# Kernel tuning notes

Measured on AMD Instinct MI355X. Metric: run time of the kernel, lower is better.

The kernel has to match this reference:

```python
import jax, jax.numpy as jnp
import numpy as np

INPUT_SIZE = 4096
OUTPUT_SIZE = 4096
N = 6  # LUT fan-in -> 2^N = 64 entries per LUT
BATCH = 2048


def setup_inputs() -> dict:
    key = jax.random.key(0)
    kx, km, kl = jax.random.split(key, 3)
    # binary input bits stored as float32 {0,1}
    x = jax.random.randint(kx, (BATCH, INPUT_SIZE), 0, 2).astype(jnp.float32)
    # 'random' layer mapping: each of the OUTPUT_SIZE LUTs reads N input bit positions
    mapping = jax.random.randint(km, (OUTPUT_SIZE, N), 0, INPUT_SIZE).astype(jnp.int32)
    # LUT weights, uniform in [-1, 1] as in torch init (clamped to [-1,1] anyway)
    luts = jax.random.uniform(kl, (OUTPUT_SIZE, 2 ** N), dtype=jnp.float32) * 2.0 - 1.0
    return {"x": x, "mapping": mapping, "luts": luts}


def _lut_forward(x, mapping, luts):
    # clamp_luts (training-time clamp, applied in-place in torch forward)
    luts = jnp.clip(luts, -1.0, 1.0)
    n = mapping.shape[1]
    # gather the selected input bits: (B, O, n)
    selected = x[:, mapping]
    # pack bits into a LUT address: (B, O)
    powers = (2 ** jnp.arange(n, dtype=jnp.int32)).astype(x.dtype)
    addresses = (selected * powers).sum(axis=-1).astype(jnp.int32)
    # second gather: per-output LUT lookup -> (B, O)
    out = luts[jnp.arange(luts.shape[0], dtype=jnp.int32)[None, :], addresses]
    # STE binarization (forward: hard threshold > 0)
    binary = (out > 0).astype(out.dtype)
    return out + jax.lax.stop_gradient(binary - out) if False else binary  # fwd-only: hard output


def reference(x, mapping, luts):
    return _lut_forward(x, mapping, luts)
```

## Files before the change

### kernel.cpp

```cpp
#include <hip/hip_runtime.h>
#include <stdint.h>


static constexpr int IN    = 4096;
static constexpr int OUTW  = 4096;
static constexpr int BATCH = 2048;

__global__ __launch_bounds__(256) void prep_kernel(const float* __restrict__ x,
                                                   const float* __restrict__ luts,
                                                   uint32_t* __restrict__ xbits,
                                                   unsigned long long* __restrict__ lut_pos) {
    if (blockIdx.x < 256) {
        const int g = blockIdx.x >> 2;
        const int chunk = blockIdx.x & 3;
        const int m = chunk * 1024 + threadIdx.x * 4;
        const float* xb = x + ((size_t)g * 32) * IN + m;
        uint32_t v0 = 0, v1 = 0, v2 = 0, v3 = 0;
#pragma unroll
        for (int r = 0; r < 32; ++r) {
            const float4 f = *(const float4*)(xb + (size_t)r * IN);
            v0 |= ((uint32_t)(f.x != 0.0f)) << r;
            v1 |= ((uint32_t)(f.y != 0.0f)) << r;
            v2 |= ((uint32_t)(f.z != 0.0f)) << r;
            v3 |= ((uint32_t)(f.w != 0.0f)) << r;
        }
        *(uint4*)(xbits + (size_t)g * IN + m) = make_uint4(v0, v1, v2, v3);
    } else {
        const int wave = threadIdx.x >> 6;
        const int lane = threadIdx.x & 63;
        const int base = (blockIdx.x - 256) * 128 + wave * 32;
#pragma unroll
        for (int i = 0; i < 32; i += 4) {
            const float v0 = luts[(size_t)(base + i + 0) * 64 + lane];
            const float v1 = luts[(size_t)(base + i + 1) * 64 + lane];
            const float v2 = luts[(size_t)(base + i + 2) * 64 + lane];
            const float v3 = luts[(size_t)(base + i + 3) * 64 + lane];
            const unsigned long long m0 = __ballot(v0 > 0.0f);
            const unsigned long long m1 = __ballot(v1 > 0.0f);
            const unsigned long long m2 = __ballot(v2 > 0.0f);
            const unsigned long long m3 = __ballot(v3 > 0.0f);
            if (lane == 0) {
                lut_pos[base + i + 0] = m0;
                lut_pos[base + i + 1] = m1;
                lut_pos[base + i + 2] = m2;
                lut_pos[base + i + 3] = m3;
            }
        }
    }
}

__global__ __launch_bounds__(256) void lut_fwd_kernel(const int* __restrict__ mapping,
                                                      const uint32_t* __restrict__ xbits,
                                                      const unsigned long long* __restrict__ lut_pos,
                                                      float* __restrict__ out) {
    __shared__ uint32_t sbits[IN];
    const int g  = blockIdx.x & 63;
    const int cb = blockIdx.x >> 6;
    {
        const uint4* src = (const uint4*)(xbits + (size_t)g * IN);
        uint4* dst = (uint4*)sbits;
#pragma unroll
        for (int i = 0; i < 4; ++i) dst[threadIdx.x + i * 256] = src[threadIdx.x + i * 256];
    }
    __syncthreads();

    const int j = cb * 512 + threadIdx.x * 2;
    const int4* mrow = (const int4*)(mapping + (size_t)j * 6);
    const int4 q0 = mrow[0];
    const int4 q1 = mrow[1];
    const int4 q2 = mrow[2];

    const uint32_t w00 = sbits[q0.x], w01 = sbits[q0.y], w02 = sbits[q0.z],
                   w03 = sbits[q0.w], w04 = sbits[q1.x], w05 = sbits[q1.y];
    const uint32_t w10 = sbits[q1.z], w11 = sbits[q1.w], w12 = sbits[q2.x],
                   w13 = sbits[q2.y], w14 = sbits[q2.z], w15 = sbits[q2.w];
    const ulonglong2 masks = *(const ulonglong2*)(lut_pos + j);

    float* outp = out + ((size_t)g * 32) * OUTW + j;
#pragma unroll
    for (int r = 0; r < 32; ++r) {
        const uint32_t a0 = ((w00 >> r) & 1u)        | (((w01 >> r) & 1u) << 1)
                          | (((w02 >> r) & 1u) << 2) | (((w03 >> r) & 1u) << 3)
                          | (((w04 >> r) & 1u) << 4) | (((w05 >> r) & 1u) << 5);
        const uint32_t a1 = ((w10 >> r) & 1u)        | (((w11 >> r) & 1u) << 1)
                          | (((w12 >> r) & 1u) << 2) | (((w13 >> r) & 1u) << 3)
                          | (((w14 >> r) & 1u) << 4) | (((w15 >> r) & 1u) << 5);
        float2 res;
        res.x = (float)((uint32_t)(masks.x >> a0) & 1u);
        res.y = (float)((uint32_t)(masks.y >> a1) & 1u);
        *(float2*)(outp + (size_t)r * OUTW) = res;
    }
}

__global__ __launch_bounds__(256) void naive_kernel(const float* __restrict__ x,
                                                    const int* __restrict__ mapping,
                                                    const float* __restrict__ luts,
                                                    float* __restrict__ out) {
    const int idx = blockIdx.x * 256 + threadIdx.x;
    const int b = idx >> 12;
    const int j = idx & (OUTW - 1);
    const float* xr = x + (size_t)b * IN;
    int addr = 0;
#pragma unroll
    for (int k = 0; k < 6; ++k) {
        addr |= ((int)(xr[mapping[j * 6 + k]] != 0.0f)) << k;
    }
    out[idx] = (luts[j * 64 + addr] > 0.0f) ? 1.0f : 0.0f;
}

extern "C" void kernel_launch(void* const* d_in, const int* in_sizes, int n_in,
                              void* d_out, int out_size, void* d_ws, size_t ws_size,
                              hipStream_t stream) {
    const float* x       = (const float*)d_in[0];
    const int*   mapping = (const int*)d_in[1];
    const float* luts    = (const float*)d_in[2];
    float* out = (float*)d_out;

    const size_t lut_pos_bytes = (size_t)OUTW * 8;
    const size_t xbits_bytes   = (size_t)64 * IN * 4;
    if (ws_size >= lut_pos_bytes + xbits_bytes) {
        unsigned long long* lut_pos = (unsigned long long*)d_ws;
        uint32_t* xbits = (uint32_t*)((char*)d_ws + lut_pos_bytes);
        hipLaunchKernelGGL(prep_kernel, dim3(288), dim3(256), 0, stream,
                           x, luts, xbits, lut_pos);
        hipLaunchKernelGGL(lut_fwd_kernel, dim3(512), dim3(256), 0, stream,
                           mapping, xbits, lut_pos, out);
    } else {
        hipLaunchKernelGGL(naive_kernel, dim3((BATCH * OUTW) / 256), dim3(256), 0, stream,
                           x, mapping, luts, out);
    }
}
```

Measured before the change: 91.48 us.

## Fuse bit-packing, LUT mask prep and lookup into a single kernel

Replaces the prep kernel plus lookup kernel with one kernel. Each block packs its batch group's input bits and computes the LUT sign masks for its output chunk directly into shared memory, then produces its outputs with nontemporal stores. This removes the second launch and the workspace round-trip. In exchange, each batch group's x slice is re-read by four blocks, LUT data is recomputed per block, and the grid is small (256 blocks of 512 threads).

```diff
diff --git a/kernel.cpp b/kernel.cpp
--- a/kernel.cpp
+++ b/kernel.cpp
@@ -6,14 +6,23 @@
 static constexpr int OUTW  = 4096;
 static constexpr int BATCH = 2048;
 
-__global__ __launch_bounds__(256) void prep_kernel(const float* __restrict__ x,
-                                                   const float* __restrict__ luts,
-                                                   uint32_t* __restrict__ xbits,
-                                                   unsigned long long* __restrict__ lut_pos) {
-    if (blockIdx.x < 256) {
-        const int g = blockIdx.x >> 2;
-        const int chunk = blockIdx.x & 3;
-        const int m = chunk * 1024 + threadIdx.x * 4;
+typedef float vfloat2 __attribute__((ext_vector_type(2)));
+
+__global__ __launch_bounds__(512) void fused_kernel(const float* __restrict__ x,
+                                                    const int* __restrict__ mapping,
+                                                    const float* __restrict__ luts,
+                                                    float* __restrict__ out) {
+    __shared__ uint32_t sbits[IN];
+    __shared__ unsigned long long smask[1024];
+
+    const int bid  = blockIdx.x;
+    const int slot = bid >> 3;
+    const int g    = (bid & 7) * 8 + (slot >> 2);
+    const int cb   = slot & 3;
+
+#pragma unroll
+    for (int c = 0; c < 2; ++c) {
+        const int m = c * 2048 + threadIdx.x * 4;
         const float* xb = x + ((size_t)g * 32) * IN + m;
         uint32_t v0 = 0, v1 = 0, v2 = 0, v3 = 0;
 #pragma unroll
@@ -24,47 +33,36 @@
             v2 |= ((uint32_t)(f.z != 0.0f)) << r;
             v3 |= ((uint32_t)(f.w != 0.0f)) << r;
         }
-        *(uint4*)(xbits + (size_t)g * IN + m) = make_uint4(v0, v1, v2, v3);
-    } else {
-        const int wave = threadIdx.x >> 6;
-        const int lane = threadIdx.x & 63;
-        const int base = (blockIdx.x - 256) * 128 + wave * 32;
+        *(uint4*)(sbits + m) = make_uint4(v0, v1, v2, v3);
+    }
+
+    {
+        const int wave  = threadIdx.x >> 6;
+        const int lane  = threadIdx.x & 63;
+        const int cbase = wave * 128;
+        const float* lp = luts + ((size_t)(cb * 1024 + cbase)) * 64 + lane;
 #pragma unroll
-        for (int i = 0; i < 32; i += 4) {
-            const float v0 = luts[(size_t)(base + i + 0) * 64 + lane];
-            const float v1 = luts[(size_t)(base + i + 1) * 64 + lane];
-            const float v2 = luts[(size_t)(base + i + 2) * 64 + lane];
-            const float v3 = luts[(size_t)(base + i + 3) * 64 + lane];
+        for (int i = 0; i < 128; i += 4) {
+            const float v0 = lp[(size_t)(i + 0) * 64];
+            const float v1 = lp[(size_t)(i + 1) * 64];
+            const float v2 = lp[(size_t)(i + 2) * 64];
+            const float v3 = lp[(size_t)(i + 3) * 64];
             const unsigned long long m0 = __ballot(v0 > 0.0f);
             const unsigned long long m1 = __ballot(v1 > 0.0f);
             const unsigned long long m2 = __ballot(v2 > 0.0f);
             const unsigned long long m3 = __ballot(v3 > 0.0f);
             if (lane == 0) {
-                lut_pos[base + i + 0] = m0;
-                lut_pos[base + i + 1] = m1;
-                lut_pos[base + i + 2] = m2;
-                lut_pos[base + i + 3] = m3;
+                smask[cbase + i + 0] = m0;
+                smask[cbase + i + 1] = m1;
+                smask[cbase + i + 2] = m2;
+                smask[cbase + i + 3] = m3;
             }
         }
     }
-}
-
-__global__ __launch_bounds__(256) void lut_fwd_kernel(const int* __restrict__ mapping,
-                                                      const uint32_t* __restrict__ xbits,
-                                                      const unsigned long long* __restrict__ lut_pos,
-                                                      float* __restrict__ out) {
-    __shared__ uint32_t sbits[IN];
-    const int g  = blockIdx.x & 63;
-    const int cb = blockIdx.x >> 6;
-    {
-        const uint4* src = (const uint4*)(xbits + (size_t)g * IN);
-        uint4* dst = (uint4*)sbits;
-#pragma unroll
-        for (int i = 0; i < 4; ++i) dst[threadIdx.x + i * 256] = src[threadIdx.x + i * 256];
-    }
     __syncthreads();
 
-    const int j = cb * 512 + threadIdx.x * 2;
+    const int jl = threadIdx.x * 2;
+    const int j  = cb * 1024 + jl;
     const int4* mrow = (const int4*)(mapping + (size_t)j * 6);
     const int4 q0 = mrow[0];
     const int4 q1 = mrow[1];
@@ -74,7 +72,8 @@
                    w03 = sbits[q0.w], w04 = sbits[q1.x], w05 = sbits[q1.y];
     const uint32_t w10 = sbits[q1.z], w11 = sbits[q1.w], w12 = sbits[q2.x],
                    w13 = sbits[q2.y], w14 = sbits[q2.z], w15 = sbits[q2.w];
-    const ulonglong2 masks = *(const ulonglong2*)(lut_pos + j);
+    const unsigned long long mk0 = smask[jl];
+    const unsigned long long mk1 = smask[jl + 1];
 
     float* outp = out + ((size_t)g * 32) * OUTW + j;
 #pragma unroll
@@ -85,27 +84,11 @@
         const uint32_t a1 = ((w10 >> r) & 1u)        | (((w11 >> r) & 1u) << 1)
                           | (((w12 >> r) & 1u) << 2) | (((w13 >> r) & 1u) << 3)
                           | (((w14 >> r) & 1u) << 4) | (((w15 >> r) & 1u) << 5);
-        float2 res;
-        res.x = (float)((uint32_t)(masks.x >> a0) & 1u);
-        res.y = (float)((uint32_t)(masks.y >> a1) & 1u);
-        *(float2*)(outp + (size_t)r * OUTW) = res;
+        vfloat2 res;
+        res.x = (float)((uint32_t)(mk0 >> a0) & 1u);
+        res.y = (float)((uint32_t)(mk1 >> a1) & 1u);
+        __builtin_nontemporal_store(res, (vfloat2*)(outp + (size_t)r * OUTW));
     }
-}
-
-__global__ __launch_bounds__(256) void naive_kernel(const float* __restrict__ x,
-                                                    const int* __restrict__ mapping,
-                                                    const float* __restrict__ luts,
-                                                    float* __restrict__ out) {
-    const int idx = blockIdx.x * 256 + threadIdx.x;
-    const int b = idx >> 12;
-    const int j = idx & (OUTW - 1);
-    const float* xr = x + (size_t)b * IN;
-    int addr = 0;
-#pragma unroll
-    for (int k = 0; k < 6; ++k) {
-        addr |= ((int)(xr[mapping[j * 6 + k]] != 0.0f)) << k;
-    }
-    out[idx] = (luts[j * 64 + addr] > 0.0f) ? 1.0f : 0.0f;
 }
 
 extern "C" void kernel_launch(void* const* d_in, const int* in_sizes, int n_in,
@@ -115,18 +98,8 @@
     const int*   mapping = (const int*)d_in[1];
     const float* luts    = (const float*)d_in[2];
     float* out = (float*)d_out;
+    (void)d_ws; (void)ws_size;
 
-    const size_t lut_pos_bytes = (size_t)OUTW * 8;
-    const size_t xbits_bytes   = (size_t)64 * IN * 4;
-    if (ws_size >= lut_pos_bytes + xbits_bytes) {
-        unsigned long long* lut_pos = (unsigned long long*)d_ws;
-        uint32_t* xbits = (uint32_t*)((char*)d_ws + lut_pos_bytes);
-        hipLaunchKernelGGL(prep_kernel, dim3(288), dim3(256), 0, stream,
-                           x, luts, xbits, lut_pos);
-        hipLaunchKernelGGL(lut_fwd_kernel, dim3(512), dim3(256), 0, stream,
-                           mapping, xbits, lut_pos, out);
-    } else {
-        hipLaunchKernelGGL(naive_kernel, dim3((BATCH * OUTW) / 256), dim3(256), 0, stream,
-                           x, mapping, luts, out);
-    }
+    hipLaunchKernelGGL(fused_kernel, dim3(256), dim3(512), 0, stream,
+                       x, mapping, luts, out);
 }
```

After: 99.43 us. 1.09x slower.

## Fuse x bit-packing into main kernel, 4 rows per block, nontemporal IO

Applied to the files above, without the earlier changes.

Moves the packing of input bits into the main kernel. Each block now packs 4 batch rows straight into shared memory, which removes the xbits workspace round trip and its separate launch. The LUT sign-mask prep becomes its own small kernel. Each thread now handles 4 outputs per row with float4 nontemporal stores and nontemporal loads of x. The trade-off is that every block now reloads all 4096 mapping entries and lut masks for only 4 rows, where before it reused them across 32 rows, so mapping and mask traffic per output rises.

```diff
diff --git a/kernel.cpp b/kernel.cpp
--- a/kernel.cpp
+++ b/kernel.cpp
@@ -6,89 +6,102 @@
 static constexpr int OUTW  = 4096;
 static constexpr int BATCH = 2048;
 
-__global__ __launch_bounds__(256) void prep_kernel(const float* __restrict__ x,
-                                                   const float* __restrict__ luts,
-                                                   uint32_t* __restrict__ xbits,
-                                                   unsigned long long* __restrict__ lut_pos) {
-    if (blockIdx.x < 256) {
-        const int g = blockIdx.x >> 2;
-        const int chunk = blockIdx.x & 3;
-        const int m = chunk * 1024 + threadIdx.x * 4;
-        const float* xb = x + ((size_t)g * 32) * IN + m;
+typedef float vfloat4 __attribute__((ext_vector_type(4)));
+
+__global__ __launch_bounds__(256) void lutprep_kernel(const float* __restrict__ luts,
+                                                      unsigned long long* __restrict__ lut_pos) {
+    const int wave = threadIdx.x >> 6;
+    const int lane = threadIdx.x & 63;
+    const int base = blockIdx.x * 256 + wave * 64;
+#pragma unroll
+    for (int i = 0; i < 64; i += 4) {
+        const float v0 = luts[(size_t)(base + i + 0) * 64 + lane];
+        const float v1 = luts[(size_t)(base + i + 1) * 64 + lane];
+        const float v2 = luts[(size_t)(base + i + 2) * 64 + lane];
+        const float v3 = luts[(size_t)(base + i + 3) * 64 + lane];
+        const unsigned long long m0 = __ballot(v0 > 0.0f);
+        const unsigned long long m1 = __ballot(v1 > 0.0f);
+        const unsigned long long m2 = __ballot(v2 > 0.0f);
+        const unsigned long long m3 = __ballot(v3 > 0.0f);
+        if (lane == 0) {
+            lut_pos[base + i + 0] = m0;
+            lut_pos[base + i + 1] = m1;
+            lut_pos[base + i + 2] = m2;
+            lut_pos[base + i + 3] = m3;
+        }
+    }
+}
+
+__global__ __launch_bounds__(256) void lut_main_kernel(const float* __restrict__ x,
+                                                       const int* __restrict__ mapping,
+                                                       const unsigned long long* __restrict__ lut_pos,
+                                                       float* __restrict__ out) {
+    __shared__ uint32_t sbits[IN];
+    const int g = blockIdx.x;
+    const int t = threadIdx.x;
+
+#pragma unroll
+    for (int c = 0; c < 4; ++c) {
+        const int m = c * 1024 + t * 4;
+        const float* xb = x + ((size_t)g * 4) * IN + m;
         uint32_t v0 = 0, v1 = 0, v2 = 0, v3 = 0;
 #pragma unroll
-        for (int r = 0; r < 32; ++r) {
-            const float4 f = *(const float4*)(xb + (size_t)r * IN);
+        for (int r = 0; r < 4; ++r) {
+            const vfloat4 f = __builtin_nontemporal_load((const vfloat4*)(xb + (size_t)r * IN));
             v0 |= ((uint32_t)(f.x != 0.0f)) << r;
             v1 |= ((uint32_t)(f.y != 0.0f)) << r;
             v2 |= ((uint32_t)(f.z != 0.0f)) << r;
             v3 |= ((uint32_t)(f.w != 0.0f)) << r;
         }
-        *(uint4*)(xbits + (size_t)g * IN + m) = make_uint4(v0, v1, v2, v3);
-    } else {
-        const int wave = threadIdx.x >> 6;
-        const int lane = threadIdx.x & 63;
-        const int base = (blockIdx.x - 256) * 128 + wave * 32;
-#pragma unroll
-        for (int i = 0; i < 32; i += 4) {
-            const float v0 = luts[(size_t)(base + i + 0) * 64 + lane];
-            const float v1 = luts[(size_t)(base + i + 1) * 64 + lane];
-            const float v2 = luts[(size_t)(base + i + 2) * 64 + lane];
-            const float v3 = luts[(size_t)(base + i + 3) * 64 + lane];
-            const unsigned long long m0 = __ballot(v0 > 0.0f);
-            const unsigned long long m1 = __ballot(v1 > 0.0f);
-            const unsigned long long m2 = __ballot(v2 > 0.0f);
-            const unsigned long long m3 = __ballot(v3 > 0.0f);
-            if (lane == 0) {
-                lut_pos[base + i + 0] = m0;
-                lut_pos[base + i + 1] = m1;
-                lut_pos[base + i + 2] = m2;
-                lut_pos[base + i + 3] = m3;
-            }
-        }
-    }
-}
-
-__global__ __launch_bounds__(256) void lut_fwd_kernel(const int* __restrict__ mapping,
-                                                      const uint32_t* __restrict__ xbits,
-                                                      const unsigned long long* __restrict__ lut_pos,
-                                                      float* __restrict__ out) {
-    __shared__ uint32_t sbits[IN];
-    const int g  = blockIdx.x & 63;
-    const int cb = blockIdx.x >> 6;
-    {
-        const uint4* src = (const uint4*)(xbits + (size_t)g * IN);
-        uint4* dst = (uint4*)sbits;
-#pragma unroll
-        for (int i = 0; i < 4; ++i) dst[threadIdx.x + i * 256] = src[threadIdx.x + i * 256];
+        *(uint4*)(sbits + m) = make_uint4(v0, v1, v2, v3);
     }
     __syncthreads();
 
-    const int j = cb * 512 + threadIdx.x * 2;
-    const int4* mrow = (const int4*)(mapping + (size_t)j * 6);
-    const int4 q0 = mrow[0];
-    const int4 q1 = mrow[1];
-    const int4 q2 = mrow[2];
+#pragma unroll
+    for (int c = 0; c < 4; ++c) {
+        const int j = c * 1024 + t * 4;
+        const int4* mrow = (const int4*)(mapping + (size_t)j * 6);
+        const int4 q0 = mrow[0];
+        const int4 q1 = mrow[1];
+        const int4 q2 = mrow[2];
+        const int4 q3 = mrow[3];
+        const int4 q4 = mrow[4];
+        const int4 q5 = mrow[5];
 
-    const uint32_t w00 = sbits[q0.x], w01 = sbits[q0.y], w02 = sbits[q0.z],
-                   w03 = sbits[q0.w], w04 = sbits[q1.x], w05 = sbits[q1.y];
-    const uint32_t w10 = sbits[q1.z], w11 = sbits[q1.w], w12 = sbits[q2.x],
-                   w13 = sbits[q2.y], w14 = sbits[q2.z], w15 = sbits[q2.w];
-    const ulonglong2 masks = *(const ulonglong2*)(lut_pos + j);
+        const uint32_t w00 = sbits[q0.x], w01 = sbits[q0.y], w02 = sbits[q0.z],
+                       w03 = sbits[q0.w], w04 = sbits[q1.x], w05 = sbits[q1.y];
+        const uint32_t w10 = sbits[q1.z], w11 = sbits[q1.w], w12 = sbits[q2.x],
+                       w13 = sbits[q2.y], w14 = sbits[q2.z], w15 = sbits[q2.w];
+        const uint32_t w20 = sbits[q3.x], w21 = sbits[q3.y], w22 = sbits[q3.z],
+                       w23 = sbits[q3.w], w24 = sbits[q4.x], w25 = sbits[q4.y];
+        const uint32_t w30 = sbits[q4.z], w31 = sbits[q4.w], w32 = sbits[q5.x],
+                       w33 = sbits[q5.y], w34 = sbits[q5.z], w35 = sbits[q5.w];
 
-    float* outp = out + ((size_t)g * 32) * OUTW + j;
+        const ulonglong2 mk01 = *(const ulonglong2*)(lut_pos + j);
+        const ulonglong2 mk23 = *(const ulonglong2*)(lut_pos + j + 2);
+
+        float* outp = out + ((size_t)g * 4) * OUTW + j;
 #pragma unroll
-    for (int r = 0; r < 32; ++r) {
-        const uint32_t a0 = ((w00 >> r) & 1u)        | (((w01 >> r) & 1u) << 1)
-                          | (((w02 >> r) & 1u) << 2) | (((w03 >> r) & 1u) << 3)
-                          | (((w04 >> r) & 1u) << 4) | (((w05 >> r) & 1u) << 5);
-        const uint32_t a1 = ((w10 >> r) & 1u)        | (((w11 >> r) & 1u) << 1)
-                          | (((w12 >> r) & 1u) << 2) | (((w13 >> r) & 1u) << 3)
-                          | (((w14 >> r) & 1u) << 4) | (((w15 >> r) & 1u) << 5);
-        float2 res;
-        res.x = (float)((uint32_t)(masks.x >> a0) & 1u);
-        res.y = (float)((uint32_t)(masks.y >> a1) & 1u);
-        *(float2*)(outp + (size_t)r * OUTW) = res;
+        for (int r = 0; r < 4; ++r) {
+            const uint32_t a0 = ((w00 >> r) & 1u)        | (((w01 >> r) & 1u) << 1)
+                              | (((w02 >> r) & 1u) << 2) | (((w03 >> r) & 1u) << 3)
+                              | (((w04 >> r) & 1u) << 4) | (((w05 >> r) & 1u) << 5);
+            const uint32_t a1 = ((w10 >> r) & 1u)        | (((w11 >> r) & 1u) << 1)
+                              | (((w12 >> r) & 1u) << 2) | (((w13 >> r) & 1u) << 3)
+                              | (((w14 >> r) & 1u) << 4) | (((w15 >> r) & 1u) << 5);
+            const uint32_t a2 = ((w20 >> r) & 1u)        | (((w21 >> r) & 1u) << 1)
+                              | (((w22 >> r) & 1u) << 2) | (((w23 >> r) & 1u) << 3)
+                              | (((w24 >> r) & 1u) << 4) | (((w25 >> r) & 1u) << 5);
+            const uint32_t a3 = ((w30 >> r) & 1u)        | (((w31 >> r) & 1u) << 1)
+                              | (((w32 >> r) & 1u) << 2) | (((w33 >> r) & 1u) << 3)
+                              | (((w34 >> r) & 1u) << 4) | (((w35 >> r) & 1u) << 5);
+            vfloat4 res;
+            res.x = (float)((uint32_t)(mk01.x >> a0) & 1u);
+            res.y = (float)((uint32_t)(mk01.y >> a1) & 1u);
+            res.z = (float)((uint32_t)(mk23.x >> a2) & 1u);
+            res.w = (float)((uint32_t)(mk23.y >> a3) & 1u);
+            __builtin_nontemporal_store(res, (vfloat4*)(outp + (size_t)r * OUTW));
+        }
     }
 }
 
@@ -97,6 +110,7 @@
                                                     const float* __restrict__ luts,
                                                     float* __restrict__ out) {
     const int idx = blockIdx.x * 256 + threadIdx.x;
+    if (idx >= BATCH * OUTW) return;
     const int b = idx >> 12;
     const int j = idx & (OUTW - 1);
     const float* xr = x + (size_t)b * IN;
@@ -117,14 +131,12 @@
     float* out = (float*)d_out;
 
     const size_t lut_pos_bytes = (size_t)OUTW * 8;
-    const size_t xbits_bytes   = (size_t)64 * IN * 4;
-    if (ws_size >= lut_pos_bytes + xbits_bytes) {
+    if (ws_size >= lut_pos_bytes) {
         unsigned long long* lut_pos = (unsigned long long*)d_ws;
-        uint32_t* xbits = (uint32_t*)((char*)d_ws + lut_pos_bytes);
-        hipLaunchKernelGGL(prep_kernel, dim3(288), dim3(256), 0, stream,
-                           x, luts, xbits, lut_pos);
-        hipLaunchKernelGGL(lut_fwd_kernel, dim3(512), dim3(256), 0, stream,
-                           mapping, xbits, lut_pos, out);
+        hipLaunchKernelGGL(lutprep_kernel, dim3(16), dim3(256), 0, stream,
+                           luts, lut_pos);
+        hipLaunchKernelGGL(lut_main_kernel, dim3(512), dim3(256), 0, stream,
+                           x, mapping, lut_pos, out);
     } else {
         hipLaunchKernelGGL(naive_kernel, dim3((BATCH * OUTW) / 256), dim3(256), 0, stream,
                            x, mapping, luts, out);
```

Result: slower. 98.47 us (+7.6%).
